# Kernel optimization log

Measured on AMD Instinct MI355X. Metric: run time of the kernel, lower is better.

The kernel has to match this reference:

```python
import jax, jax.numpy as jnp
import numpy as np

DIM = 768
NUM_HEADS = 12
HEAD_DIM = DIM // NUM_HEADS
EPS = 1e-5


def setup_inputs() -> dict:
    key = jax.random.key(0)
    ks = jax.random.split(key, 12)
    s = 0.02
    return {
        "x": jax.random.normal(ks[0], (8, 1024, DIM), jnp.float32),
        "pos_embed": jax.random.normal(ks[1], (8, 1024, DIM), jnp.float32),
        "gamma": jnp.ones((DIM,), jnp.float32),
        "beta": jnp.zeros((DIM,), jnp.float32),
        "Wq": jax.random.normal(ks[2], (DIM, DIM), jnp.float32) * s,
        "bq": jnp.zeros((DIM,), jnp.float32),
        "Wk": jax.random.normal(ks[3], (DIM, DIM), jnp.float32) * s,
        "bk": jnp.zeros((DIM,), jnp.float32),
        "Wv": jax.random.normal(ks[4], (DIM, DIM), jnp.float32) * s,
        "bv": jnp.zeros((DIM,), jnp.float32),
        "Wo": jax.random.normal(ks[5], (DIM, DIM), jnp.float32) * s,
        "bo": jnp.zeros((DIM,), jnp.float32),
    }


def _split_heads(t):
    B, N, C = t.shape
    return t.reshape(B, N, NUM_HEADS, HEAD_DIM).transpose(0, 2, 1, 3)  # (B,H,N,D)


def reference(x, pos_embed, gamma, beta, Wq, bq, Wk, bk, Wv, bv, Wo, bo):
    B, N, C = x.shape
    # pre-LayerNorm
    mu = jnp.mean(x, axis=-1, keepdims=True)
    var = jnp.mean(jnp.square(x - mu), axis=-1, keepdims=True)
    x_norm = (x - mu) * jax.lax.rsqrt(var + EPS) * gamma + beta

    Q = _split_heads(x_norm @ Wq + bq) + _split_heads(pos_embed)  # pos-embed added to Q
    K = _split_heads(x_norm @ Wk + bk)
    V = _split_heads(x_norm @ Wv + bv)

    inv_temp = 1.0 / jnp.sqrt(jnp.float32(HEAD_DIM))
    S = jnp.einsum("bhnd,bhmd->bhnm", Q, K) * inv_temp  # (B,H,N,N)
    A = jax.nn.softmax(S, axis=-1)  # dropout p=0.0 -> identity
    vals = jnp.einsum("bhnm,bhmd->bhnd", A, V)
    vals = vals.transpose(0, 2, 1, 3).reshape(B, N, C)
    return vals @ Wo + bo + x  # residual
```

## Files before the change

### kernel.cpp

```cpp
#include <hip/hip_runtime.h>
#include <hip/hip_bf16.h>

#define TOK 8192
#define CDIM 768
#define NH 12
#define HD 64
#define QKV_N 2304
#define QSCALE 0.18033688011f
#define MREF 10.0f

typedef __attribute__((ext_vector_type(8))) short bf16x8;
typedef __attribute__((ext_vector_type(4))) float f32x4;
typedef unsigned short ushort_t;

__device__ __forceinline__ ushort_t f2bf(float f) {
  unsigned u = __float_as_uint(f);
  u += 0x7fffu + ((u >> 16) & 1u);
  return (ushort_t)(u >> 16);
}

__device__ __forceinline__ f32x4 mfma16(bf16x8 a, bf16x8 b, f32x4 c) {
  return __builtin_amdgcn_mfma_f32_16x16x32_bf16(a, b, c, 0, 0, 0);
}

__device__ __forceinline__ int swz(int r) { return (r ^ (r >> 3)) & 7; }

__device__ __forceinline__ void gload16(const void* g, void* l) {
  __builtin_amdgcn_global_load_lds(
      (const __attribute__((address_space(1))) unsigned int*)g,
      (__attribute__((address_space(3))) unsigned int*)l, 16, 0, 0);
}

__global__ __launch_bounds__(256) void ln_kernel(const float* __restrict__ x,
                                                 const float* __restrict__ gamma,
                                                 const float* __restrict__ beta,
                                                 ushort_t* __restrict__ xn) {
  int t = blockIdx.x;
  const float* row = x + (size_t)t * CDIM;
  float v[3];
  float s = 0.f, s2 = 0.f;
#pragma unroll
  for (int i = 0; i < 3; i++) {
    v[i] = row[threadIdx.x + 256 * i];
    s += v[i];
    s2 += v[i] * v[i];
  }
#pragma unroll
  for (int off = 32; off; off >>= 1) {
    s += __shfl_xor(s, off);
    s2 += __shfl_xor(s2, off);
  }
  __shared__ float red[8];
  int wid = threadIdx.x >> 6, lane = threadIdx.x & 63;
  if (lane == 0) { red[wid] = s; red[wid + 4] = s2; }
  __syncthreads();
  s = red[0] + red[1] + red[2] + red[3];
  s2 = red[4] + red[5] + red[6] + red[7];
  float mu = s * (1.f / CDIM);
  float var = s2 * (1.f / CDIM) - mu * mu;
  float rstd = rsqrtf(var + 1e-5f);
  ushort_t* orow = xn + (size_t)t * CDIM;
#pragma unroll
  for (int i = 0; i < 3; i++) {
    int c = threadIdx.x + 256 * i;
    orow[c] = f2bf((v[i] - mu) * rstd * gamma[c] + beta[c]);
  }
}

__global__ __launch_bounds__(256) void wtrans_kernel(const float* __restrict__ Wq,
                                                     const float* __restrict__ Wk,
                                                     const float* __restrict__ Wv,
                                                     const float* __restrict__ Wo,
                                                     ushort_t* __restrict__ wt) {
  const float* W = (blockIdx.z == 0) ? Wq : (blockIdx.z == 1) ? Wk
                   : (blockIdx.z == 2) ? Wv : Wo;
  __shared__ float tile[32][33];
  int tr = blockIdx.y, tc = blockIdx.x;
  int tx = threadIdx.x, ty = threadIdx.y;
#pragma unroll
  for (int j = 0; j < 4; j++) {
    int k = tr * 32 + ty + j * 8;
    tile[ty + j * 8][tx] = W[(size_t)k * CDIM + tc * 32 + tx];
  }
  __syncthreads();
  ushort_t* o = wt + (size_t)blockIdx.z * CDIM * CDIM;
#pragma unroll
  for (int j = 0; j < 4; j++) {
    int n = tc * 32 + ty + j * 8;
    o[(size_t)n * CDIM + tr * 32 + tx] = f2bf(tile[tx][ty + j * 8]);
  }
}

__global__ __launch_bounds__(512) void gemm0_kernel(
    const ushort_t* __restrict__ A, const ushort_t* __restrict__ Bt,
    const float* __restrict__ bq, const float* __restrict__ bk,
    const float* __restrict__ bv, const float* __restrict__ pos,
    ushort_t* __restrict__ outp) {
  __shared__ __align__(16) ushort_t lds_a[2][256 * 64];
  __shared__ __align__(16) ushort_t lds_b[2][256 * 64];
  int lin = blockIdx.y * 9 + blockIdx.x;
  int nl = (lin & 7) * 36 + (lin >> 3);
  const int bn = nl % 9, bm = nl / 9;

  const int tid = threadIdx.x;
  const int lane = tid & 63, wid = tid >> 6;
  const int wr = wid >> 2, wc = wid & 3;
  const int l16 = lane & 15, lg = lane >> 4;
  f32x4 acc[8][4] = {};

  int aoff[2][8], boff[2][4];
#pragma unroll
  for (int kk = 0; kk < 2; kk++) {
#pragma unroll
    for (int mi = 0; mi < 8; mi++) {
      int r = wr * 128 + mi * 16 + l16;
      aoff[kk][mi] = r * 64 + (((kk * 4 + lg) ^ swz(r)) & 7) * 8;
    }
#pragma unroll
    for (int ni = 0; ni < 4; ni++) {
      int r = wc * 64 + ni * 16 + l16;
      boff[kk][ni] = r * 64 + (((kk * 4 + lg) ^ swz(r)) & 7) * 8;
    }
  }

  auto stageA = [&](int buf, int k0, int u) {
    int s = u * 512 + tid;
    int row = s >> 3, j = s & 7;
    int c8 = ((j ^ swz(row)) & 7) * 8;
    gload16(&A[(size_t)(bm * 256 + row) * CDIM + k0 + c8], &lds_a[buf][s * 8]);
  };
  auto stageB = [&](int buf, int k0, int u) {
    int s = u * 512 + tid;
    int row = s >> 3, j = s & 7;
    int c8 = ((j ^ swz(row)) & 7) * 8;
    gload16(&Bt[(size_t)(bn * 256 + row) * CDIM + k0 + c8], &lds_b[buf][s * 8]);
  };

#pragma unroll
  for (int u = 0; u < 4; u++) { stageA(0, 0, u); stageB(0, 0, u); }
  asm volatile("s_waitcnt vmcnt(0)" ::: "memory");
  __builtin_amdgcn_s_barrier();

  int cur = 0;
  for (int t = 0; t < 12; t++) {
    const int k0n = (t + 1) * 64;
    const bool st = (t < 11);
    bf16x8 bf[2][4];
#pragma unroll
    for (int kk = 0; kk < 2; kk++)
#pragma unroll
      for (int ni = 0; ni < 4; ni++)
        bf[kk][ni] = *reinterpret_cast<const bf16x8*>(&lds_b[cur][boff[kk][ni]]);

#pragma unroll
    for (int p = 0; p < 4; p++) {
      if (st) { stageA(cur ^ 1, k0n, p); stageB(cur ^ 1, k0n, p); }
      bf16x8 af[2][2];
#pragma unroll
      for (int kk = 0; kk < 2; kk++)
#pragma unroll
        for (int q = 0; q < 2; q++)
          af[kk][q] = *reinterpret_cast<const bf16x8*>(
              &lds_a[cur][aoff[kk][2 * p + q]]);
      __builtin_amdgcn_s_setprio(1);
#pragma unroll
      for (int kk = 0; kk < 2; kk++)
#pragma unroll
        for (int q = 0; q < 2; q++)
#pragma unroll
          for (int ni = 0; ni < 4; ni++)
            acc[2 * p + q][ni] = mfma16(af[kk][q], bf[kk][ni], acc[2 * p + q][ni]);
      __builtin_amdgcn_s_setprio(0);
    }
    asm volatile("s_waitcnt vmcnt(0) lgkmcnt(0)" ::: "memory");
    __builtin_amdgcn_s_barrier();
    cur ^= 1;
  }

#pragma unroll
  for (int mi = 0; mi < 8; mi++)
#pragma unroll
    for (int ni = 0; ni < 4; ni++)
#pragma unroll
      for (int r = 0; r < 4; r++) {
        int grow = bm * 256 + wr * 128 + mi * 16 + 4 * lg + r;
        int gcol = bn * 256 + wc * 64 + ni * 16 + l16;
        float v = acc[mi][ni][r];
        if (gcol < 768) {
          v = (v + bq[gcol] + pos[(size_t)grow * CDIM + gcol]) * QSCALE;
        } else if (gcol < 1536) {
          v += bk[gcol - 768];
        } else {
          v += bv[gcol - 1536];
        }
        outp[(size_t)grow * QKV_N + gcol] = f2bf(v);
      }
}

__global__ __launch_bounds__(256) void gemm1_kernel(
    const ushort_t* __restrict__ A, const ushort_t* __restrict__ Bt,
    const float* __restrict__ b0, const float* __restrict__ extra,
    float* __restrict__ outp) {
  __shared__ __align__(16) ushort_t lds_a[2][128 * 64];
  __shared__ __align__(16) ushort_t lds_b[2][128 * 64];
  const int NB = 6;
  int lin = blockIdx.y * NB + blockIdx.x;
  int nl = (lin & 7) * (NB * 8) + (lin >> 3);
  const int bn = nl % NB, bm = nl / NB;

  const int tid = threadIdx.x;
  const int lane = tid & 63, wid = tid >> 6;
  const int wr = wid >> 1, wc = wid & 1;
  const int l16 = lane & 15, lg = lane >> 4;
  f32x4 acc[4][4] = {};

  int aoff[2][4], boff[2][4];
#pragma unroll
  for (int kk = 0; kk < 2; kk++) {
#pragma unroll
    for (int mi = 0; mi < 4; mi++) {
      int r = wr * 64 + mi * 16 + l16;
      aoff[kk][mi] = r * 64 + (((kk * 4 + lg) ^ swz(r)) & 7) * 8;
    }
#pragma unroll
    for (int ni = 0; ni < 4; ni++) {
      int r = wc * 64 + ni * 16 + l16;
      boff[kk][ni] = r * 64 + (((kk * 4 + lg) ^ swz(r)) & 7) * 8;
    }
  }

  auto stage = [&](int buf, int k0) {
#pragma unroll
    for (int i = 0; i < 4; i++) {
      int slot = i * 256 + tid;
      int row = slot >> 3, j = slot & 7;
      int c8 = ((j ^ swz(row)) & 7) * 8;
      gload16(&A[(size_t)(bm * 128 + row) * CDIM + k0 + c8], &lds_a[buf][slot * 8]);
      gload16(&Bt[(size_t)(bn * 128 + row) * CDIM + k0 + c8], &lds_b[buf][slot * 8]);
    }
  };

  stage(0, 0);
  asm volatile("s_waitcnt vmcnt(0)" ::: "memory");
  __builtin_amdgcn_s_barrier();
  __builtin_amdgcn_sched_barrier(0);

  int cur = 0;
#pragma unroll 2
  for (int t = 0; t < 12; t++) {
    if (t < 11) stage(cur ^ 1, (t + 1) * 64);
#pragma unroll
    for (int kk = 0; kk < 2; kk++) {
      bf16x8 af[4], bfr[4];
#pragma unroll
      for (int mi = 0; mi < 4; mi++)
        af[mi] = *reinterpret_cast<const bf16x8*>(&lds_a[cur][aoff[kk][mi]]);
#pragma unroll
      for (int ni = 0; ni < 4; ni++)
        bfr[ni] = *reinterpret_cast<const bf16x8*>(&lds_b[cur][boff[kk][ni]]);
      __builtin_amdgcn_s_setprio(1);
#pragma unroll
      for (int mi = 0; mi < 4; mi++)
#pragma unroll
        for (int ni = 0; ni < 4; ni++)
          acc[mi][ni] = mfma16(af[mi], bfr[ni], acc[mi][ni]);
      __builtin_amdgcn_s_setprio(0);
    }
    asm volatile("s_waitcnt vmcnt(0) lgkmcnt(0)" ::: "memory");
    __builtin_amdgcn_s_barrier();
    __builtin_amdgcn_sched_barrier(0);
    cur ^= 1;
  }

#pragma unroll
  for (int mi = 0; mi < 4; mi++)
#pragma unroll
    for (int ni = 0; ni < 4; ni++)
#pragma unroll
      for (int r = 0; r < 4; r++) {
        int grow = bm * 128 + wr * 64 + mi * 16 + 4 * lg + r;
        int gcol = bn * 128 + wc * 64 + ni * 16 + l16;
        outp[(size_t)grow * CDIM + gcol] =
            acc[mi][ni][r] + b0[gcol] + extra[(size_t)grow * CDIM + gcol];
      }
}

__global__ __launch_bounds__(256, 3) void attn_kernel(const ushort_t* __restrict__ QKV,
                                                      ushort_t* __restrict__ O) {
  const int b = blockIdx.x, h = blockIdx.y, qt = blockIdx.z;

  const int tid = threadIdx.x, lane = tid & 63, w = tid >> 6;
  const int l16 = lane & 15, lg = lane >> 4;
  const int tb = b * 1024 + qt * 128;
  const int co_q = h * HD, co_k = CDIM + h * HD, co_v = 2 * CDIM + h * HD;

  __shared__ __align__(16) ushort_t k_lds[2][64 * 64];
  __shared__ __align__(16) ushort_t vt_lds[2][64 * 64];
  __shared__ __align__(16) ushort_t p_lds[128 * 64];

  bf16x8 qf[2][2];
#pragma unroll
  for (int mi = 0; mi < 2; mi++)
#pragma unroll
    for (int ds = 0; ds < 2; ds++)
      qf[mi][ds] = *reinterpret_cast<const bf16x8*>(
          &QKV[(size_t)(tb + w * 32 + mi * 16 + l16) * QKV_N + co_q + ds * 32 + 8 * lg]);

  float m_sm[2] = {MREF, MREF};
  float l_sm[2] = {0.f, 0.f};
  float m_acc[2][4];
#pragma unroll
  for (int mi = 0; mi < 2; mi++)
#pragma unroll
    for (int r = 0; r < 4; r++) m_acc[mi][r] = MREF;
  f32x4 oacc[2][4] = {};

  int kfoff[2][4];
#pragma unroll
  for (int ds = 0; ds < 2; ds++)
#pragma unroll
    for (int ni = 0; ni < 4; ni++) {
      int rr = ni * 16 + l16;
      kfoff[ds][ni] = rr * 64 + (((ds * 4 + lg) ^ swz(rr)) & 7) * 8;
    }
  int poff[2][4], paoff[2][2];
#pragma unroll
  for (int mi = 0; mi < 2; mi++) {
    int myq = w * 32 + mi * 16 + l16;
    int sq = swz(myq);
#pragma unroll
    for (int ni = 0; ni < 4; ni++)
      poff[mi][ni] = myq * 64 + (lg & 1) * 4 + (((ni * 2 + (lg >> 1)) ^ sq) & 7) * 8;
#pragma unroll
    for (int ks = 0; ks < 2; ks++)
      paoff[mi][ks] = myq * 64 + (((ks * 4 + lg) ^ sq) & 7) * 8;
  }
  int vboff[2][4];
#pragma unroll
  for (int ks = 0; ks < 2; ks++)
#pragma unroll
    for (int ni = 0; ni < 4; ni++) {
      int d = ni * 16 + l16;
      vboff[ks][ni] = d * 64 + (((ks * 4 + lg) ^ swz(d)) & 7) * 8;
    }

  auto stage_k = [&](int buf, int kt) {
    const int kv0 = kt * 64;
#pragma unroll
    for (int i = 0; i < 2; i++) {
      int slot = i * 256 + tid;
      int r = slot >> 3, j = slot & 7;
      int c = ((j ^ swz(r)) & 7) * 8;
      gload16(&QKV[(size_t)(b * 1024 + kv0 + r) * QKV_N + co_k + c],
              &k_lds[buf][slot * 8]);
    }
  };

  const int kv0 = (tid >> 3) * 2, d0 = (tid & 7) * 8;
  const int sV = ((kv0 >> 3) ^ (d0 >> 3)) & 7;
  int voff[8];
#pragma unroll
  for (int u = 0; u < 8; u++)
    voff[u] = (d0 + u) * 64 + ((sV ^ u) & 7) * 8 + (kv0 & 7);
  const ushort_t* vsrc = QKV + (size_t)(b * 1024 + kv0) * QKV_N + co_v + d0;

  uint4 vr0, vr1;
  auto load_v = [&](int kt) {
    vr0 = *reinterpret_cast<const uint4*>(vsrc + (size_t)kt * 64 * QKV_N);
    vr1 = *reinterpret_cast<const uint4*>(vsrc + (size_t)kt * 64 * QKV_N + QKV_N);
  };
  auto write_v = [&](int buf) {
    const unsigned* w0 = reinterpret_cast<const unsigned*>(&vr0);
    const unsigned* w1 = reinterpret_cast<const unsigned*>(&vr1);
#pragma unroll
    for (int u = 0; u < 8; u++) {
      unsigned a = w0[u >> 1], c = w1[u >> 1];
      unsigned val = (u & 1) ? ((a >> 16) | (c & 0xffff0000u))
                             : ((a & 0xffffu) | (c << 16));
      *reinterpret_cast<unsigned*>(&vt_lds[buf][voff[u]]) = val;
    }
  };

  stage_k(0, 0);
  load_v(0);
  write_v(0);
  asm volatile("s_waitcnt vmcnt(0) lgkmcnt(0)" ::: "memory");
  __builtin_amdgcn_s_barrier();
  __builtin_amdgcn_sched_barrier(0);

  for (int kt = 0; kt < 16; kt++) {
    const int cur = kt & 1, nxt = cur ^ 1;
    if (kt < 15) { stage_k(nxt, kt + 1); load_v(kt + 1); }

    bf16x8 kf[2][4];
#pragma unroll
    for (int ds = 0; ds < 2; ds++)
#pragma unroll
      for (int ni = 0; ni < 4; ni++)
        kf[ds][ni] = *reinterpret_cast<const bf16x8*>(&k_lds[cur][kfoff[ds][ni]]);

#pragma unroll
    for (int mi = 0; mi < 2; mi++) {
      f32x4 st[4] = {};
      __builtin_amdgcn_s_setprio(1);
#pragma unroll
      for (int ds = 0; ds < 2; ds++)
#pragma unroll
        for (int ni = 0; ni < 4; ni++)
          st[ni] = mfma16(kf[ds][ni], qf[mi][ds], st[ni]);
      __builtin_amdgcn_s_setprio(0);

      float t0 = fmaxf(fmaxf(st[0][0], st[0][1]), fmaxf(st[0][2], st[0][3]));
      float t1 = fmaxf(fmaxf(st[1][0], st[1][1]), fmaxf(st[1][2], st[1][3]));
      float t2 = fmaxf(fmaxf(st[2][0], st[2][1]), fmaxf(st[2][2], st[2][3]));
      float t3 = fmaxf(fmaxf(st[3][0], st[3][1]), fmaxf(st[3][2], st[3][3]));
      float tm = fmaxf(fmaxf(t0, t1), fmaxf(t2, t3));

      if (__any(tm > m_sm[mi])) {
        float rm = fmaxf(tm, __shfl_xor(tm, 16));
        rm = fmaxf(rm, __shfl_xor(rm, 32));
        float mnew = fmaxf(m_sm[mi], rm);
        l_sm[mi] *= exp2f(m_sm[mi] - mnew);
        m_sm[mi] = mnew;
#pragma unroll
        for (int r = 0; r < 4; r++) {
          float mn = __shfl(mnew, 4 * lg + r);
          float corr = exp2f(m_acc[mi][r] - mn);
          m_acc[mi][r] = mn;
#pragma unroll
          for (int ni = 0; ni < 4; ni++) oacc[mi][ni][r] *= corr;
        }
      }

      float ps[4];
#pragma unroll
      for (int ni = 0; ni < 4; ni++) {
        float e0 = exp2f(st[ni][0] - m_sm[mi]);
        float e1 = exp2f(st[ni][1] - m_sm[mi]);
        float e2 = exp2f(st[ni][2] - m_sm[mi]);
        float e3 = exp2f(st[ni][3] - m_sm[mi]);
        st[ni][0] = e0; st[ni][1] = e1; st[ni][2] = e2; st[ni][3] = e3;
        ps[ni] = (e0 + e1) + (e2 + e3);
      }
      l_sm[mi] += (ps[0] + ps[1]) + (ps[2] + ps[3]);

#pragma unroll
      for (int ni = 0; ni < 4; ni++) {
        unsigned p01, p23;
        asm("v_cvt_pk_bf16_f32 %0, %1, %2" : "=v"(p01) : "v"(st[ni][0]), "v"(st[ni][1]));
        asm("v_cvt_pk_bf16_f32 %0, %1, %2" : "=v"(p23) : "v"(st[ni][2]), "v"(st[ni][3]));
        uint2 pk; pk.x = p01; pk.y = p23;
        *reinterpret_cast<uint2*>(&p_lds[poff[mi][ni]]) = pk;
      }
    }

#pragma unroll
    for (int ks = 0; ks < 2; ks++) {
      bf16x8 pa0 = *reinterpret_cast<const bf16x8*>(&p_lds[paoff[0][ks]]);
      bf16x8 pa1 = *reinterpret_cast<const bf16x8*>(&p_lds[paoff[1][ks]]);
      bf16x8 vb[4];
#pragma unroll
      for (int ni = 0; ni < 4; ni++)
        vb[ni] = *reinterpret_cast<const bf16x8*>(&vt_lds[cur][vboff[ks][ni]]);
      __builtin_amdgcn_s_setprio(1);
#pragma unroll
      for (int ni = 0; ni < 4; ni++) {
        oacc[0][ni] = mfma16(pa0, vb[ni], oacc[0][ni]);
        oacc[1][ni] = mfma16(pa1, vb[ni], oacc[1][ni]);
      }
      __builtin_amdgcn_s_setprio(0);
    }

    if (kt < 15) write_v(nxt);
    asm volatile("s_waitcnt vmcnt(0) lgkmcnt(0)" ::: "memory");
    __builtin_amdgcn_s_barrier();
    __builtin_amdgcn_sched_barrier(0);
  }

#pragma unroll
  for (int mi = 0; mi < 2; mi++) {
    float l = l_sm[mi];
    l += __shfl_xor(l, 16);
    l += __shfl_xor(l, 32);
#pragma unroll
    for (int r = 0; r < 4; r++) {
      float lr = __shfl(l, 4 * lg + r);
      float inv = 1.f / lr;
      int grow = tb + w * 32 + mi * 16 + 4 * lg + r;
#pragma unroll
      for (int ni = 0; ni < 4; ni++) {
        int gcol = h * HD + ni * 16 + l16;
        O[(size_t)grow * CDIM + gcol] = f2bf(oacc[mi][ni][r] * inv);
      }
    }
  }
}

extern "C" void kernel_launch(void* const* d_in, const int* in_sizes, int n_in,
                              void* d_out, int out_size, void* d_ws, size_t ws_size,
                              hipStream_t stream) {
  const float* x     = (const float*)d_in[0];
  const float* pos   = (const float*)d_in[1];
  const float* gamma = (const float*)d_in[2];
  const float* beta  = (const float*)d_in[3];
  const float* Wq    = (const float*)d_in[4];
  const float* bq    = (const float*)d_in[5];
  const float* Wk    = (const float*)d_in[6];
  const float* bk    = (const float*)d_in[7];
  const float* Wv    = (const float*)d_in[8];
  const float* bv    = (const float*)d_in[9];
  const float* Wo    = (const float*)d_in[10];
  const float* bo    = (const float*)d_in[11];
  float* out = (float*)d_out;

  ushort_t* xn   = (ushort_t*)d_ws;
  ushort_t* wt   = xn + (size_t)TOK * CDIM;
  ushort_t* qkv  = wt + (size_t)3072 * CDIM;
  ushort_t* aout = qkv + (size_t)TOK * QKV_N;

  ln_kernel<<<TOK, 256, 0, stream>>>(x, gamma, beta, xn);
  wtrans_kernel<<<dim3(24, 24, 4), dim3(32, 8), 0, stream>>>(Wq, Wk, Wv, Wo, wt);
  gemm0_kernel<<<dim3(9, 32), 512, 0, stream>>>(xn, wt, bq, bk, bv, pos, qkv);
  attn_kernel<<<dim3(8, NH, 8), 256, 0, stream>>>(qkv, aout);
  gemm1_kernel<<<dim3(6, 64), 256, 0, stream>>>(aout, wt + (size_t)QKV_N * CDIM,
                                                bo, x, out);
}
```

Baseline: 186.6 us.

## Split QKV GEMM K-tiles into half-tiles with finer-grained staged prefetch pipeline

Measured after the change: 185.6 us. No clear change (-0.5%).

```diff
diff --git a/kernel.cpp b/kernel.cpp
--- a/kernel.cpp
+++ b/kernel.cpp
@@ -96,8 +96,8 @@
     const float* __restrict__ bq, const float* __restrict__ bk,
     const float* __restrict__ bv, const float* __restrict__ pos,
     ushort_t* __restrict__ outp) {
-  __shared__ __align__(16) ushort_t lds_a[2][256 * 64];
-  __shared__ __align__(16) ushort_t lds_b[2][256 * 64];
+  __shared__ __align__(16) ushort_t lds_a[2][2 * 256 * 32];
+  __shared__ __align__(16) ushort_t lds_b[2][2 * 256 * 32];
   int lin = blockIdx.y * 9 + blockIdx.x;
   int nl = (lin & 7) * 36 + (lin >> 3);
   const int bn = nl % 9, bm = nl / 9;
@@ -113,67 +113,128 @@
   for (int kk = 0; kk < 2; kk++) {
 #pragma unroll
     for (int mi = 0; mi < 8; mi++) {
-      int r = wr * 128 + mi * 16 + l16;
-      aoff[kk][mi] = r * 64 + (((kk * 4 + lg) ^ swz(r)) & 7) * 8;
+      int ra = wr * 128 + mi * 16 + l16;
+      aoff[kk][mi] = kk * 8192 + ra * 32 + ((lg ^ ((ra >> 1) & 3)) & 3) * 8;
     }
 #pragma unroll
     for (int ni = 0; ni < 4; ni++) {
-      int r = wc * 64 + ni * 16 + l16;
-      boff[kk][ni] = r * 64 + (((kk * 4 + lg) ^ swz(r)) & 7) * 8;
-    }
-  }
-
-  auto stageA = [&](int buf, int k0, int u) {
-    int s = u * 512 + tid;
-    int row = s >> 3, j = s & 7;
-    int c8 = ((j ^ swz(row)) & 7) * 8;
-    gload16(&A[(size_t)(bm * 256 + row) * CDIM + k0 + c8], &lds_a[buf][s * 8]);
+      int rb = wc * 64 + ni * 16 + l16;
+      boff[kk][ni] = kk * 8192 + rb * 32 + ((lg ^ ((rb >> 1) & 3)) & 3) * 8;
+    }
+  }
+
+  auto stA = [&](int buf, int t, int kk) {
+#pragma unroll
+    for (int u = 0; u < 2; u++) {
+      int s = u * 512 + tid;
+      int row = s >> 2, j = s & 3;
+      int c8 = ((j ^ ((row >> 1) & 3)) & 3) * 8;
+      gload16(&A[(size_t)(bm * 256 + row) * CDIM + t * 64 + kk * 32 + c8],
+              &lds_a[buf][kk * 8192 + s * 8]);
+    }
   };
-  auto stageB = [&](int buf, int k0, int u) {
-    int s = u * 512 + tid;
-    int row = s >> 3, j = s & 7;
-    int c8 = ((j ^ swz(row)) & 7) * 8;
-    gload16(&Bt[(size_t)(bn * 256 + row) * CDIM + k0 + c8], &lds_b[buf][s * 8]);
+  auto stB = [&](int buf, int t, int kk) {
+#pragma unroll
+    for (int u = 0; u < 2; u++) {
+      int s = u * 512 + tid;
+      int row = s >> 2, j = s & 3;
+      int c8 = ((j ^ ((row >> 1) & 3)) & 3) * 8;
+      gload16(&Bt[(size_t)(bn * 256 + row) * CDIM + t * 64 + kk * 32 + c8],
+              &lds_b[buf][kk * 8192 + s * 8]);
+    }
   };
 
-#pragma unroll
-  for (int u = 0; u < 4; u++) { stageA(0, 0, u); stageB(0, 0, u); }
-  asm volatile("s_waitcnt vmcnt(0)" ::: "memory");
+  stA(0, 0, 0); stB(0, 0, 0); stA(0, 0, 1); stB(0, 0, 1);
+  asm volatile("s_waitcnt vmcnt(4)" ::: "memory");
   __builtin_amdgcn_s_barrier();
+  __builtin_amdgcn_sched_barrier(0);
 
   int cur = 0;
   for (int t = 0; t < 12; t++) {
-    const int k0n = (t + 1) * 64;
+    const int nxt = cur ^ 1;
     const bool st = (t < 11);
-    bf16x8 bf[2][4];
-#pragma unroll
-    for (int kk = 0; kk < 2; kk++)
-#pragma unroll
-      for (int ni = 0; ni < 4; ni++)
-        bf[kk][ni] = *reinterpret_cast<const bf16x8*>(&lds_b[cur][boff[kk][ni]]);
-
-#pragma unroll
-    for (int p = 0; p < 4; p++) {
-      if (st) { stageA(cur ^ 1, k0n, p); stageB(cur ^ 1, k0n, p); }
-      bf16x8 af[2][2];
-#pragma unroll
-      for (int kk = 0; kk < 2; kk++)
-#pragma unroll
-        for (int q = 0; q < 2; q++)
-          af[kk][q] = *reinterpret_cast<const bf16x8*>(
-              &lds_a[cur][aoff[kk][2 * p + q]]);
-      __builtin_amdgcn_s_setprio(1);
-#pragma unroll
-      for (int kk = 0; kk < 2; kk++)
-#pragma unroll
-        for (int q = 0; q < 2; q++)
-#pragma unroll
-          for (int ni = 0; ni < 4; ni++)
-            acc[2 * p + q][ni] = mfma16(af[kk][q], bf[kk][ni], acc[2 * p + q][ni]);
-      __builtin_amdgcn_s_setprio(0);
-    }
-    asm volatile("s_waitcnt vmcnt(0) lgkmcnt(0)" ::: "memory");
-    __builtin_amdgcn_s_barrier();
+    bf16x8 bfr[4], af[4];
+
+    if (st) stA(nxt, t + 1, 0);
+#pragma unroll
+    for (int ni = 0; ni < 4; ni++)
+      bfr[ni] = *reinterpret_cast<const bf16x8*>(&lds_b[cur][boff[0][ni]]);
+#pragma unroll
+    for (int q = 0; q < 4; q++)
+      af[q] = *reinterpret_cast<const bf16x8*>(&lds_a[cur][aoff[0][q]]);
+    __builtin_amdgcn_s_barrier();
+    asm volatile("s_waitcnt lgkmcnt(0)" ::: "memory");
+    __builtin_amdgcn_sched_barrier(0);
+    __builtin_amdgcn_s_setprio(1);
+#pragma unroll
+    for (int q = 0; q < 4; q++)
+#pragma unroll
+      for (int ni = 0; ni < 4; ni++)
+        acc[q][ni] = mfma16(af[q], bfr[ni], acc[q][ni]);
+    __builtin_amdgcn_s_setprio(0);
+    __builtin_amdgcn_s_barrier();
+    __builtin_amdgcn_sched_barrier(0);
+
+    if (st) stB(nxt, t + 1, 0);
+#pragma unroll
+    for (int q = 0; q < 4; q++)
+      af[q] = *reinterpret_cast<const bf16x8*>(&lds_a[cur][aoff[0][4 + q]]);
+    __builtin_amdgcn_s_barrier();
+    asm volatile("s_waitcnt lgkmcnt(0)" ::: "memory");
+    __builtin_amdgcn_sched_barrier(0);
+    __builtin_amdgcn_s_setprio(1);
+#pragma unroll
+    for (int q = 0; q < 4; q++)
+#pragma unroll
+      for (int ni = 0; ni < 4; ni++)
+        acc[4 + q][ni] = mfma16(af[q], bfr[ni], acc[4 + q][ni]);
+    __builtin_amdgcn_s_setprio(0);
+    if (t < 11)
+      asm volatile("s_waitcnt vmcnt(4)" ::: "memory");
+    else
+      asm volatile("s_waitcnt vmcnt(0)" ::: "memory");
+    __builtin_amdgcn_s_barrier();
+    __builtin_amdgcn_sched_barrier(0);
+
+    if (st) stA(nxt, t + 1, 1);
+#pragma unroll
+    for (int ni = 0; ni < 4; ni++)
+      bfr[ni] = *reinterpret_cast<const bf16x8*>(&lds_b[cur][boff[1][ni]]);
+#pragma unroll
+    for (int q = 0; q < 4; q++)
+      af[q] = *reinterpret_cast<const bf16x8*>(&lds_a[cur][aoff[1][q]]);
+    __builtin_amdgcn_s_barrier();
+    asm volatile("s_waitcnt lgkmcnt(0)" ::: "memory");
+    __builtin_amdgcn_sched_barrier(0);
+    __builtin_amdgcn_s_setprio(1);
+#pragma unroll
+    for (int q = 0; q < 4; q++)
+#pragma unroll
+      for (int ni = 0; ni < 4; ni++)
+        acc[q][ni] = mfma16(af[q], bfr[ni], acc[q][ni]);
+    __builtin_amdgcn_s_setprio(0);
+    __builtin_amdgcn_s_barrier();
+    __builtin_amdgcn_sched_barrier(0);
+
+    if (st) stB(nxt, t + 1, 1);
+#pragma unroll
+    for (int q = 0; q < 4; q++)
+      af[q] = *reinterpret_cast<const bf16x8*>(&lds_a[cur][aoff[1][4 + q]]);
+    __builtin_amdgcn_s_barrier();
+    asm volatile("s_waitcnt lgkmcnt(0)" ::: "memory");
+    __builtin_amdgcn_sched_barrier(0);
+    __builtin_amdgcn_s_setprio(1);
+#pragma unroll
+    for (int q = 0; q < 4; q++)
+#pragma unroll
+      for (int ni = 0; ni < 4; ni++)
+        acc[4 + q][ni] = mfma16(af[q], bfr[ni], acc[4 + q][ni]);
+    __builtin_amdgcn_s_setprio(0);
+    if (t < 11)
+      asm volatile("s_waitcnt vmcnt(4)" ::: "memory");
+    __builtin_amdgcn_s_barrier();
+    __builtin_amdgcn_sched_barrier(0);
+
     cur ^= 1;
   }
 
```
